# Kernel optimization log

Measured on AMD Instinct MI355X. Metric: run time of the kernel, lower is better.

Reference implementation:

```python
import jax, jax.numpy as jnp
import numpy as np

SCORE_THRESHOLD = 0.15
IOU_THRESHOLD = 0.5
MAX_OUTPUT = 10          # tf.image.non_max_suppression(..., 10, ...)
NUM_CLASSES = 80
NUM_ANCHORS = 5
NEG = -1e9               # score for suppressed / below-threshold boxes


def setup_inputs() -> dict:
    key = jax.random.key(0)
    k1, k2 = jax.random.split(key)
    preds = jax.random.normal(k1, (16, 52, 52, NUM_ANCHORS * (5 + NUM_CLASSES)), dtype=jnp.float32)
    # anchor priors in grid-cell units, typical YOLOv2 range
    anchors = jax.random.uniform(k2, (NUM_ANCHORS, 2), dtype=jnp.float32, minval=0.5, maxval=6.0)
    return {"preds": preds, "anchors": anchors}


def _decode(preds, anchors):
    """YOLOv2 head decode (the `_interpret_prediction` callable)."""
    B, H, W, _ = preds.shape
    A = anchors.shape[0]
    p = preds.reshape(B, H, W, A, 5 + NUM_CLASSES)
    gy, gx = jnp.meshgrid(jnp.arange(H, dtype=preds.dtype),
                          jnp.arange(W, dtype=preds.dtype), indexing="ij")
    grid = jnp.stack([gx, gy], axis=-1)[None, :, :, None, :]   # (1,H,W,1,2) in (x,y)
    dims = jnp.array([W, H], dtype=preds.dtype)
    box_xy = (jax.nn.sigmoid(p[..., :2]) + grid) / dims        # normalized centers
    box_wh = jnp.exp(p[..., 2:4]) * anchors[None, None, None, :, :] / dims
    box_confidence = jax.nn.sigmoid(p[..., 4:5])
    box_class_probs = jax.nn.softmax(p[..., 5:], axis=-1)
    return box_xy, box_wh, box_confidence, box_class_probs


def _iou(box, boxes):
    """IoU of one box (ymin,xmin,ymax,xmax) against all boxes [N,4]."""
    tl = jnp.maximum(box[:2], boxes[:, :2])
    br = jnp.minimum(box[2:], boxes[:, 2:])
    inter = jnp.prod(jnp.maximum(br - tl, 0.0), axis=-1)
    area1 = jnp.prod(jnp.maximum(box[2:] - box[:2], 0.0))
    area2 = jnp.prod(jnp.maximum(boxes[:, 2:] - boxes[:, :2], 0.0), axis=-1)
    return inter / (area1 + area2 - inter + 1e-9)


def reference(preds, anchors):
    box_xy, box_wh, box_confidence, box_class_probs = _decode(preds, anchors)
    box_mins = box_xy - box_wh / 2.0
    box_maxes = box_xy + box_wh / 2.0
    # (ymin, xmin, ymax, xmax), matching the K.concatenate in the source
    boxes = jnp.concatenate([box_mins[..., 1:2], box_mins[..., 0:1],
                             box_maxes[..., 1:2], box_maxes[..., 0:1]], axis=-1)
    box_scores = box_confidence * box_class_probs
    box_classes = jnp.argmax(box_scores, axis=-1)
    box_class_scores = jnp.max(box_scores, axis=-1)

    boxes = boxes.reshape(-1, 4)                       # [N,4]
    scores = box_class_scores.reshape(-1)              # [N]
    classes = box_classes.reshape(-1).astype(preds.dtype)

    # score-threshold mask: instead of boolean_mask (dynamic shape), kill scores
    live = jnp.where(scores >= SCORE_THRESHOLD, scores, NEG)

    # greedy NMS, fixed MAX_OUTPUT iterations (semantics of tf.image.non_max_suppression)
    def step(cur_scores, _):
        i = jnp.argmax(cur_scores)
        s = cur_scores[i]
        valid = s > NEG / 2
        box = boxes[i]
        ious = _iou(box, boxes)
        nxt = jnp.where(ious > IOU_THRESHOLD, NEG, cur_scores).at[i].set(NEG)
        row = jnp.where(valid,
                        jnp.concatenate([box, s[None], classes[i][None]]),
                        jnp.zeros((6,), dtype=preds.dtype))
        return nxt, row

    _, rows = jax.lax.scan(step, live, None, length=MAX_OUTPUT)
    return rows  # [10, 6] = (ymin, xmin, ymax, xmax, score, class); zero rows = padding
```

## Files before the change

### kernel.cpp

```cpp
#include <hip/hip_runtime.h>
#include <math.h>

#define A_N      5
#define GRID_HW  52
#define NCLS     80
#define CH       85
#define SCORE_T  0.15f
#define IOU_T    0.5f
#define NEGV     (-1e9f)
#define MAXOUT   10

#define WAVES_PB     4
#define BPW          32
#define WAVE_FLOATS  (BPW * CH)
#define WAVE_FULL    10
#define WAVE_TAIL    40

#define NMS_THREADS  512
#define NWAVES       (NMS_THREADS / 64)
#define NCAP         4096
#define KR           (NCAP / NMS_THREADS)

__device__ __forceinline__ float fexp(float x) { return __expf(x); }

__device__ __forceinline__ void gload_lds16(const float* g, float* l) {
    __builtin_amdgcn_global_load_lds(
        (const __attribute__((address_space(1))) unsigned int*)g,
        (__attribute__((address_space(3))) unsigned int*)l, 16, 0, 0);
}

__global__ void init_counter_kernel(int* __restrict__ counter) {
    *counter = 0;
}

__global__ __launch_bounds__(256) void decode_kernel(
    const float* __restrict__ preds,
    const float* __restrict__ anchors,
    float4* __restrict__ pbox, float* __restrict__ pscore,
    float* __restrict__ pcls,
    int* __restrict__ counter, int N, int capacity)
{
    __shared__ __align__(16) float lds[WAVES_PB * WAVE_FLOATS];

    const int lane = (int)threadIdx.x & 63;
    const int wid  = (int)threadIdx.x >> 6;
    const int wt   = blockIdx.x * WAVES_PB + wid;
    if (wt * BPW >= N) return;

    const float* gbase = preds + (size_t)wt * WAVE_FLOATS;
    float* lbase = lds + wid * WAVE_FLOATS;

#pragma unroll
    for (int i = 0; i < WAVE_FULL; ++i)
        gload_lds16(gbase + (size_t)(i * 64 + lane) * 4, lbase + i * 256);
    if (lane < WAVE_TAIL)
        gload_lds16(gbase + (size_t)(WAVE_FULL * 64 + lane) * 4,
                    lbase + WAVE_FULL * 256);

    asm volatile("s_waitcnt vmcnt(0)" ::: "memory");
    __builtin_amdgcn_sched_barrier(0);

    const int b  = lane >> 1;
    const int h  = lane & 1;
    const int gi = wt * BPW + b;
    const float* bp = lbase + b * CH;
    const float* cl = bp + 5 + h * 40;

    float s = 0.0f;
    float m = -INFINITY;
    int   am = h * 40;
#pragma unroll
    for (int j = 0; j < 40; ++j) {
        float x = cl[j];
        s += fexp(x);
        if (x > m) { m = x; am = h * 40 + j; }
    }
    {
        float m2 = __shfl_xor(m, 1);
        float s2 = __shfl_xor(s, 1);
        int   am2 = __shfl_xor(am, 1);
        s += s2;
        if (m2 > m || (m2 == m && am2 < am)) { m = m2; am = am2; }
    }

    float conf  = 1.0f / (1.0f + fexp(-bp[4]));
    float score = conf * fexp(m) / s;

    bool live = (h == 0) && (gi < N) && (score >= SCORE_T);

    unsigned long long mask = __ballot(live);
    if (mask) {
        int nlive  = __popcll(mask);
        int leader = (int)__ffsll((long long)mask) - 1;
        int base_ = 0;
        if (lane == leader) base_ = atomicAdd(counter, nlive);
        base_ = __shfl(base_, leader);
        if (live) {
            int a = gi % A_N;
            int t = gi / A_N;
            int wx = t % GRID_HW;
            int hy = (t / GRID_HW) % GRID_HW;
            const float inv = 1.0f / (float)GRID_HW;
            float cx = (1.0f / (1.0f + fexp(-bp[0])) + (float)wx) * inv;
            float cy = (1.0f / (1.0f + fexp(-bp[1])) + (float)hy) * inv;
            float bw = fexp(bp[2]) * anchors[2 * a]     * inv;
            float bh = fexp(bp[3]) * anchors[2 * a + 1] * inv;

            int pos = base_ + __popcll(mask & ((1ull << lane) - 1));
            if (pos < capacity) {
                pbox[pos]   = make_float4(cy - 0.5f * bh, cx - 0.5f * bw,
                                          cy + 0.5f * bh, cx + 0.5f * bw);
                pscore[pos] = score;
                pcls[pos]   = (float)am;
            }
        }
    }
}

__global__ __launch_bounds__(NMS_THREADS, 1) void nms_kernel(
    const float4* __restrict__ pbox, float* __restrict__ pscore,
    const float* __restrict__ pcls, const int* __restrict__ counter,
    int capacity, float* __restrict__ pscratch, float* __restrict__ out)
{
    __shared__ float psc[NWAVES];
    __shared__ int   pix[NWAVES];
    __shared__ float orow[MAXOUT * 6];

    int M = *counter;
    if (M > capacity) M = capacity;
    const int tid  = (int)threadIdx.x;
    const int lane = tid & 63;
    const int wid  = tid >> 6;

    if (M <= NCAP) {
        float4 rb[KR];
        float  rs[KR];
#pragma unroll
        for (int k = 0; k < KR; ++k) {
            int j = tid + (k << 9);
            if (j < M) { rb[k] = pbox[j]; rs[k] = pscore[j]; }
            else       { rs[k] = -INFINITY; rb[k] = make_float4(0.f,0.f,0.f,0.f); }
        }

        for (int it = 0; it < MAXOUT; ++it) {
            float bs = -INFINITY; int bi = -1;
#pragma unroll
            for (int k = 0; k < KR; ++k) {
                if (rs[k] > bs) { bs = rs[k]; bi = tid + (k << 9); }
            }
#pragma unroll
            for (int off = 32; off; off >>= 1) {
                float os = __shfl_xor(bs, off);
                int   oi = __shfl_xor(bi, off);
                if (os > bs || (os == bs && oi != -1 && (bi == -1 || oi < bi))) {
                    bs = os; bi = oi;
                }
            }
            if (lane == 0) { psc[wid] = bs; pix[wid] = bi; }
            __syncthreads();

            bs = psc[0]; bi = pix[0];
#pragma unroll
            for (int w = 1; w < NWAVES; ++w) {
                float os = psc[w]; int oi = pix[w];
                if (os > bs || (os == bs && oi != -1 && (bi == -1 || oi < bi))) {
                    bs = os; bi = oi;
                }
            }
            bool valid = (bi >= 0) && (bs > NEGV * 0.5f);

            float4 wb = make_float4(0.f, 0.f, 0.f, 0.f);
            if (valid) wb = pbox[bi];

            if (tid == 0) {
                if (valid) {
                    orow[it*6+0] = wb.x; orow[it*6+1] = wb.y;
                    orow[it*6+2] = wb.z; orow[it*6+3] = wb.w;
                    orow[it*6+4] = bs;   orow[it*6+5] = pcls[bi];
                } else {
                    orow[it*6+0] = 0.f; orow[it*6+1] = 0.f; orow[it*6+2] = 0.f;
                    orow[it*6+3] = 0.f; orow[it*6+4] = 0.f; orow[it*6+5] = 0.f;
                }
            }

            if (valid) {
                float a1 = fmaxf(wb.z - wb.x, 0.f) * fmaxf(wb.w - wb.y, 0.f);
#pragma unroll
                for (int k = 0; k < KR; ++k) {
                    int j = tid + (k << 9);
                    if (j == bi) rs[k] = NEGV;
                    float ty = fmaxf(wb.x, rb[k].x);
                    float tx = fmaxf(wb.y, rb[k].y);
                    float by = fminf(wb.z, rb[k].z);
                    float bx = fminf(wb.w, rb[k].w);
                    float inter = fmaxf(by - ty, 0.f) * fmaxf(bx - tx, 0.f);
                    float a2 = fmaxf(rb[k].z - rb[k].x, 0.f)
                             * fmaxf(rb[k].w - rb[k].y, 0.f);
                    float iou = inter / (a1 + a2 - inter + 1e-9f);
                    if (iou > IOU_T) rs[k] = NEGV;
                }
            }
            __syncthreads();
        }
    } else {
        for (int j = tid; j < M; j += NMS_THREADS) pscratch[j] = pscore[j];
        __syncthreads();

        for (int it = 0; it < MAXOUT; ++it) {
            float bs = -INFINITY; int bi = -1;
            for (int j = tid; j < M; j += NMS_THREADS) {
                float v = pscratch[j];
                if (v > bs) { bs = v; bi = j; }
            }
#pragma unroll
            for (int off = 32; off; off >>= 1) {
                float os = __shfl_xor(bs, off);
                int   oi = __shfl_xor(bi, off);
                if (os > bs || (os == bs && oi != -1 && (bi == -1 || oi < bi))) {
                    bs = os; bi = oi;
                }
            }
            if (lane == 0) { psc[wid] = bs; pix[wid] = bi; }
            __syncthreads();
            bs = psc[0]; bi = pix[0];
#pragma unroll
            for (int w = 1; w < NWAVES; ++w) {
                float os = psc[w]; int oi = pix[w];
                if (os > bs || (os == bs && oi != -1 && (bi == -1 || oi < bi))) {
                    bs = os; bi = oi;
                }
            }
            bool valid = (bi >= 0) && (bs > NEGV * 0.5f);
            float4 wb = make_float4(0.f, 0.f, 0.f, 0.f);
            if (valid) wb = pbox[bi];
            if (tid == 0) {
                if (valid) {
                    orow[it*6+0] = wb.x; orow[it*6+1] = wb.y;
                    orow[it*6+2] = wb.z; orow[it*6+3] = wb.w;
                    orow[it*6+4] = bs;   orow[it*6+5] = pcls[bi];
                    pscratch[bi] = NEGV;
                } else {
                    orow[it*6+0] = 0.f; orow[it*6+1] = 0.f; orow[it*6+2] = 0.f;
                    orow[it*6+3] = 0.f; orow[it*6+4] = 0.f; orow[it*6+5] = 0.f;
                }
            }
            __syncthreads();
            if (valid) {
                float a1 = fmaxf(wb.z - wb.x, 0.f) * fmaxf(wb.w - wb.y, 0.f);
                for (int j = tid; j < M; j += NMS_THREADS) {
                    float4 bj = pbox[j];
                    float ty = fmaxf(wb.x, bj.x);
                    float tx = fmaxf(wb.y, bj.y);
                    float by = fminf(wb.z, bj.z);
                    float bx = fminf(wb.w, bj.w);
                    float inter = fmaxf(by - ty, 0.f) * fmaxf(bx - tx, 0.f);
                    float a2 = fmaxf(bj.z - bj.x, 0.f) * fmaxf(bj.w - bj.y, 0.f);
                    float iou = inter / (a1 + a2 - inter + 1e-9f);
                    if (iou > IOU_T) pscratch[j] = NEGV;
                }
            }
            __syncthreads();
        }
    }

    __syncthreads();
    if (tid < MAXOUT * 6) out[tid] = orow[tid];
}

extern "C" void kernel_launch(void* const* d_in, const int* in_sizes, int n_in,
                              void* d_out, int out_size, void* d_ws, size_t ws_size,
                              hipStream_t stream) {
    (void)n_in; (void)out_size;
    const float* preds   = (const float*)d_in[0];
    const float* anchors = (const float*)d_in[1];
    float* out = (float*)d_out;

    int N = in_sizes[0] / CH;

    char* ws = (char*)d_ws;
    int* counter = (int*)ws;
    size_t avail = (ws_size > 64) ? (ws_size - 64) : 0;
    long long cap = (long long)(avail / (sizeof(float4) + 3 * sizeof(float)));
    if (cap > N) cap = N;
    if (cap < 0) cap = 0;
    int capacity = (int)cap;

    float4* pbox    = (float4*)(ws + 64);
    float* pscore   = (float*)(pbox + capacity);
    float* pcls     = pscore + capacity;
    float* pscratch = pcls + capacity;

    init_counter_kernel<<<1, 1, 0, stream>>>(counter);

    int nBlocks = (N + WAVES_PB * BPW - 1) / (WAVES_PB * BPW);
    decode_kernel<<<nBlocks, 256, 0, stream>>>(
        preds, anchors, pbox, pscore, pcls, counter, N, capacity);
    nms_kernel<<<1, NMS_THREADS, 0, stream>>>(
        pbox, pscore, pcls, counter, capacity, pscratch, out);
}
```

Before: 63.06 us.

## Replace argmax-based NMS with parallel rank sort and single-wave ballot NMS

Decode now also records each candidate's global index. A multi-block rank kernel computes every candidate's sorted position by counting higher-scored entries and scatters boxes into score order. The last-arriving block (found via an atomic counter) runs greedy NMS with one wave over LDS-resident sorted boxes, using ballots over alive bitmasks to pick the next survivor instead of doing a block-wide argmax reduction with barriers each iteration. This trades per-iteration reductions and syncs for an O(M^2) rank pass, and falls back to the old scratch path when the candidate count exceeds the LDS cap, which is lower than before.

```diff
diff --git a/kernel.cpp b/kernel.cpp
--- a/kernel.cpp
+++ b/kernel.cpp
@@ -16,10 +16,10 @@
 #define WAVE_FULL    10
 #define WAVE_TAIL    40
 
-#define NMS_THREADS  512
-#define NWAVES       (NMS_THREADS / 64)
-#define NCAP         4096
-#define KR           (NCAP / NMS_THREADS)
+#define RANK_BLOCKS  32
+#define RANK_THREADS 256
+#define RCAP         2048
+#define SLOTS        32
 
 __device__ __forceinline__ float fexp(float x) { return __expf(x); }
 
@@ -29,15 +29,16 @@
         (__attribute__((address_space(3))) unsigned int*)l, 16, 0, 0);
 }
 
-__global__ void init_counter_kernel(int* __restrict__ counter) {
-    *counter = 0;
+__global__ void init_counters_kernel(int* __restrict__ counters) {
+    counters[0] = 0;
+    counters[1] = 0;
 }
 
 __global__ __launch_bounds__(256) void decode_kernel(
     const float* __restrict__ preds,
     const float* __restrict__ anchors,
     float4* __restrict__ pbox, float* __restrict__ pscore,
-    float* __restrict__ pcls,
+    float* __restrict__ pcls, int* __restrict__ pgi,
     int* __restrict__ counter, int N, int capacity)
 {
     __shared__ __align__(16) float lds[WAVES_PB * WAVE_FLOATS];
@@ -112,41 +113,137 @@
                                           cy + 0.5f * bh, cx + 0.5f * bw);
                 pscore[pos] = score;
                 pcls[pos]   = (float)am;
-            }
-        }
-    }
-}
-
-__global__ __launch_bounds__(NMS_THREADS, 1) void nms_kernel(
-    const float4* __restrict__ pbox, float* __restrict__ pscore,
-    const float* __restrict__ pcls, const int* __restrict__ counter,
-    int capacity, float* __restrict__ pscratch, float* __restrict__ out)
+                pgi[pos]    = gi;
+            }
+        }
+    }
+}
+
+__global__ __launch_bounds__(RANK_THREADS, 1) void ranknms_kernel(
+    const float4* __restrict__ pbox, const float* __restrict__ pscore,
+    const float* __restrict__ pcls, const int* __restrict__ pgi,
+    int* counters, int capacity,
+    float4* __restrict__ sbox, float* __restrict__ ssc,
+    float* __restrict__ scls, float* __restrict__ pscratch,
+    float* __restrict__ out)
 {
-    __shared__ float psc[NWAVES];
-    __shared__ int   pix[NWAVES];
+    __shared__ float l_y0[RCAP], l_x0[RCAP], l_y1[RCAP], l_x1[RCAP];
+    __shared__ float l_sc[RCAP], l_cl[RCAP];
     __shared__ float orow[MAXOUT * 6];
-
-    int M = *counter;
+    __shared__ float psc[4];
+    __shared__ int   pix[4];
+    __shared__ int   lastFlag;
+
+    const int tid = (int)threadIdx.x;
+    const int gid = (int)blockIdx.x * RANK_THREADS + tid;
+
+    int M = counters[0];
     if (M > capacity) M = capacity;
-    const int tid  = (int)threadIdx.x;
-    const int lane = tid & 63;
-    const int wid  = tid >> 6;
-
-    if (M <= NCAP) {
-        float4 rb[KR];
-        float  rs[KR];
-#pragma unroll
-        for (int k = 0; k < KR; ++k) {
-            int j = tid + (k << 9);
-            if (j < M) { rb[k] = pbox[j]; rs[k] = pscore[j]; }
-            else       { rs[k] = -INFINITY; rb[k] = make_float4(0.f,0.f,0.f,0.f); }
-        }
+
+    if (M <= RCAP && gid < M) {
+        float si = pscore[gid];
+        int   gii = pgi[gid];
+        int rank = 0;
+        int j = 0;
+        for (; j + 4 <= M; j += 4) {
+            float4 s4 = *reinterpret_cast<const float4*>(pscore + j);
+            int4   g4 = *reinterpret_cast<const int4*>(pgi + j);
+            rank += (s4.x > si) || (s4.x == si && g4.x < gii);
+            rank += (s4.y > si) || (s4.y == si && g4.y < gii);
+            rank += (s4.z > si) || (s4.z == si && g4.z < gii);
+            rank += (s4.w > si) || (s4.w == si && g4.w < gii);
+        }
+        for (; j < M; ++j) {
+            float sj = pscore[j];
+            rank += (sj > si) || (sj == si && pgi[j] < gii);
+        }
+        sbox[rank] = pbox[gid];
+        ssc[rank]  = si;
+        scls[rank] = pcls[gid];
+    }
+
+    __syncthreads();
+    if (tid == 0) {
+        __threadfence();
+        int prev = atomicAdd(counters + 1, 1);
+        lastFlag = (prev == (int)gridDim.x - 1);
+    }
+    __syncthreads();
+    if (!lastFlag) return;
+    __threadfence();
+
+    if (M <= RCAP) {
+        for (int r = tid; r < M; r += RANK_THREADS) {
+            float4 b = sbox[r];
+            l_y0[r] = b.x; l_x0[r] = b.y; l_y1[r] = b.z; l_x1[r] = b.w;
+            l_sc[r] = ssc[r]; l_cl[r] = scls[r];
+        }
+        __syncthreads();
+
+        if (tid < 64) {
+            const int lane = tid;
+            float by0[SLOTS], bx0[SLOTS], by1[SLOTS], bx1[SLOTS];
+            unsigned alive = 0u;
+#pragma unroll
+            for (int s = 0; s < SLOTS; ++s) {
+                int r = s * 64 + lane;
+                if (r < M) {
+                    by0[s] = l_y0[r]; bx0[s] = l_x0[r];
+                    by1[s] = l_y1[r]; bx1[s] = l_x1[r];
+                    alive |= (1u << s);
+                } else {
+                    by0[s] = 0.f; bx0[s] = 0.f; by1[s] = 0.f; bx1[s] = 0.f;
+                }
+            }
+
+            for (int it = 0; it < MAXOUT; ++it) {
+                int r = -1;
+                for (int s = 0; s < SLOTS; ++s) {
+                    unsigned long long mk = __ballot((alive >> s) & 1u);
+                    if (mk) { r = s * 64 + (int)__ffsll((long long)mk) - 1; break; }
+                }
+
+                if (r >= 0) {
+                    float wy0 = l_y0[r], wx0 = l_x0[r];
+                    float wy1 = l_y1[r], wx1 = l_x1[r];
+                    if (lane == 0) {
+                        orow[it*6+0] = wy0; orow[it*6+1] = wx0;
+                        orow[it*6+2] = wy1; orow[it*6+3] = wx1;
+                        orow[it*6+4] = l_sc[r]; orow[it*6+5] = l_cl[r];
+                    }
+                    if (lane == (r & 63)) alive &= ~(1u << (r >> 6));
+
+                    float a1 = fmaxf(wy1 - wy0, 0.f) * fmaxf(wx1 - wx0, 0.f);
+#pragma unroll
+                    for (int s = 0; s < SLOTS; ++s) {
+                        float ty = fmaxf(wy0, by0[s]);
+                        float tx = fmaxf(wx0, bx0[s]);
+                        float by = fminf(wy1, by1[s]);
+                        float bx = fminf(wx1, bx1[s]);
+                        float inter = fmaxf(by - ty, 0.f) * fmaxf(bx - tx, 0.f);
+                        float a2 = fmaxf(by1[s] - by0[s], 0.f)
+                                 * fmaxf(bx1[s] - bx0[s], 0.f);
+                        float iou = inter / (a1 + a2 - inter + 1e-9f);
+                        if (iou > IOU_T) alive &= ~(1u << s);
+                    }
+                } else if (lane == 0) {
+                    orow[it*6+0] = 0.f; orow[it*6+1] = 0.f; orow[it*6+2] = 0.f;
+                    orow[it*6+3] = 0.f; orow[it*6+4] = 0.f; orow[it*6+5] = 0.f;
+                }
+            }
+        }
+        __syncthreads();
+    } else {
+        const int lane = tid & 63;
+        const int wid  = tid >> 6;
+        for (int j = tid; j < M; j += RANK_THREADS) pscratch[j] = pscore[j];
+        __syncthreads();
 
         for (int it = 0; it < MAXOUT; ++it) {
             float bs = -INFINITY; int bi = -1;
-#pragma unroll
-            for (int k = 0; k < KR; ++k) {
-                if (rs[k] > bs) { bs = rs[k]; bi = tid + (k << 9); }
+            for (int j = tid; j < M; j += RANK_THREADS) {
+                float v = pscratch[j];
+                if (v > bs) { bs = v; bi = j; }
             }
 #pragma unroll
             for (int off = 32; off; off >>= 1) {
@@ -158,73 +255,9 @@
             }
             if (lane == 0) { psc[wid] = bs; pix[wid] = bi; }
             __syncthreads();
-
             bs = psc[0]; bi = pix[0];
 #pragma unroll
-            for (int w = 1; w < NWAVES; ++w) {
-                float os = psc[w]; int oi = pix[w];
-                if (os > bs || (os == bs && oi != -1 && (bi == -1 || oi < bi))) {
-                    bs = os; bi = oi;
-                }
-            }
-            bool valid = (bi >= 0) && (bs > NEGV * 0.5f);
-
-            float4 wb = make_float4(0.f, 0.f, 0.f, 0.f);
-            if (valid) wb = pbox[bi];
-
-            if (tid == 0) {
-                if (valid) {
-                    orow[it*6+0] = wb.x; orow[it*6+1] = wb.y;
-                    orow[it*6+2] = wb.z; orow[it*6+3] = wb.w;
-                    orow[it*6+4] = bs;   orow[it*6+5] = pcls[bi];
-                } else {
-                    orow[it*6+0] = 0.f; orow[it*6+1] = 0.f; orow[it*6+2] = 0.f;
-                    orow[it*6+3] = 0.f; orow[it*6+4] = 0.f; orow[it*6+5] = 0.f;
-                }
-            }
-
-            if (valid) {
-                float a1 = fmaxf(wb.z - wb.x, 0.f) * fmaxf(wb.w - wb.y, 0.f);
-#pragma unroll
-                for (int k = 0; k < KR; ++k) {
-                    int j = tid + (k << 9);
-                    if (j == bi) rs[k] = NEGV;
-                    float ty = fmaxf(wb.x, rb[k].x);
-                    float tx = fmaxf(wb.y, rb[k].y);
-                    float by = fminf(wb.z, rb[k].z);
-                    float bx = fminf(wb.w, rb[k].w);
-                    float inter = fmaxf(by - ty, 0.f) * fmaxf(bx - tx, 0.f);
-                    float a2 = fmaxf(rb[k].z - rb[k].x, 0.f)
-                             * fmaxf(rb[k].w - rb[k].y, 0.f);
-                    float iou = inter / (a1 + a2 - inter + 1e-9f);
-                    if (iou > IOU_T) rs[k] = NEGV;
-                }
-            }
-            __syncthreads();
-        }
-    } else {
-        for (int j = tid; j < M; j += NMS_THREADS) pscratch[j] = pscore[j];
-        __syncthreads();
-
-        for (int it = 0; it < MAXOUT; ++it) {
-            float bs = -INFINITY; int bi = -1;
-            for (int j = tid; j < M; j += NMS_THREADS) {
-                float v = pscratch[j];
-                if (v > bs) { bs = v; bi = j; }
-            }
-#pragma unroll
-            for (int off = 32; off; off >>= 1) {
-                float os = __shfl_xor(bs, off);
-                int   oi = __shfl_xor(bi, off);
-                if (os > bs || (os == bs && oi != -1 && (bi == -1 || oi < bi))) {
-                    bs = os; bi = oi;
-                }
-            }
-            if (lane == 0) { psc[wid] = bs; pix[wid] = bi; }
-            __syncthreads();
-            bs = psc[0]; bi = pix[0];
-#pragma unroll
-            for (int w = 1; w < NWAVES; ++w) {
+            for (int w = 1; w < 4; ++w) {
                 float os = psc[w]; int oi = pix[w];
                 if (os > bs || (os == bs && oi != -1 && (bi == -1 || oi < bi))) {
                     bs = os; bi = oi;
@@ -247,7 +280,7 @@
             __syncthreads();
             if (valid) {
                 float a1 = fmaxf(wb.z - wb.x, 0.f) * fmaxf(wb.w - wb.y, 0.f);
-                for (int j = tid; j < M; j += NMS_THREADS) {
+                for (int j = tid; j < M; j += RANK_THREADS) {
                     float4 bj = pbox[j];
                     float ty = fmaxf(wb.x, bj.x);
                     float tx = fmaxf(wb.y, bj.y);
@@ -263,7 +296,6 @@
         }
     }
 
-    __syncthreads();
     if (tid < MAXOUT * 6) out[tid] = orow[tid];
 }
 
@@ -278,23 +310,29 @@
     int N = in_sizes[0] / CH;
 
     char* ws = (char*)d_ws;
-    int* counter = (int*)ws;
+    int* counters = (int*)ws;
     size_t avail = (ws_size > 64) ? (ws_size - 64) : 0;
-    long long cap = (long long)(avail / (sizeof(float4) + 3 * sizeof(float)));
+    long long cap = (long long)(avail / 56);
     if (cap > N) cap = N;
     if (cap < 0) cap = 0;
+    cap &= ~3LL;
     int capacity = (int)cap;
 
     float4* pbox    = (float4*)(ws + 64);
-    float* pscore   = (float*)(pbox + capacity);
-    float* pcls     = pscore + capacity;
-    float* pscratch = pcls + capacity;
-
-    init_counter_kernel<<<1, 1, 0, stream>>>(counter);
+    float4* sbox    = pbox + capacity;
+    float*  pscore  = (float*)(sbox + capacity);
+    float*  pcls    = pscore + capacity;
+    int*    pgi     = (int*)(pcls + capacity);
+    float*  pscratch= (float*)(pgi + capacity);
+    float*  ssc     = pscratch + capacity;
+    float*  scls    = ssc + capacity;
+
+    init_counters_kernel<<<1, 1, 0, stream>>>(counters);
 
     int nBlocks = (N + WAVES_PB * BPW - 1) / (WAVES_PB * BPW);
     decode_kernel<<<nBlocks, 256, 0, stream>>>(
-        preds, anchors, pbox, pscore, pcls, counter, N, capacity);
-    nms_kernel<<<1, NMS_THREADS, 0, stream>>>(
-        pbox, pscore, pcls, counter, capacity, pscratch, out);
-}
+        preds, anchors, pbox, pscore, pcls, pgi, counters, N, capacity);
+    ranknms_kernel<<<RANK_BLOCKS, RANK_THREADS, 0, stream>>>(
+        pbox, pscore, pcls, pgi, counters, capacity,
+        sbox, ssc, scls, pscratch, out);
+}
```

After: 199.8 us. +216.9%, slower.
